# Performance work log

Measured on AMD Instinct MI355X. Metric: run time of the kernel, lower is better.

The kernel has to match this reference:

```python
import jax, jax.numpy as jnp
import numpy as np


def setup_inputs() -> dict:
    key = jax.random.key(0)
    k1, k2, k3 = jax.random.split(key, 3)
    B, T, N = 2, 16, 128
    INP, COND, OUT = 64, 64, 128
    x = jax.random.normal(k1, (B, T, N, INP), dtype=jnp.float32)
    cond = jax.random.normal(k2, (B, N, N, COND), dtype=jnp.float32)
    in_dim = 6 * INP + 2 * COND  # 512
    W = jax.random.normal(k3, (in_dim, OUT), dtype=jnp.float32) / np.sqrt(in_dim)
    b = jnp.zeros((OUT,), dtype=jnp.float32)
    return {"x": x, "cond": cond, "W": W, "b": b}


def reference(x, cond, W, b):
    # x: (B,T,N,C), cond: (B,N,N,Cc), W: (6C+2Cc, O), b: (O,)
    B, T, N, C = x.shape
    Cc = cond.shape[-1]
    # temporal boundary-zeroed copies (faithful to torch cat of zeros + slices)
    x1 = x.at[:, 0].set(0.0)        # zeros at t=0
    x2 = x.at[:, -1].set(0.0)       # zeros at t=T-1
    xc = jnp.concatenate([x1, x, x2], axis=-1)  # (B,T,N,3C)
    # decompose the big linear over the concat [x1_pair, x2_pair, cond1, cond2]
    W1 = W[: 3 * C]
    W2 = W[3 * C: 6 * C]
    Wc1 = W[6 * C: 6 * C + Cc]
    Wc2 = W[6 * C + Cc:]
    a = jnp.einsum('btnc,co->btno', xc, W1)               # n1 contribution
    bpart = jnp.einsum('btnc,co->btno', xc, W2)            # n2 contribution
    # cond1[b,t,i,j] = cond[b,i,j]; cond2[b,t,i,j] = cond[b,j,i]
    cpart = (jnp.einsum('bijc,co->bijo', cond, Wc1)
             + jnp.einsum('bjic,co->bijo', cond, Wc2))     # (B,N,N,O)
    s = (a[:, :, :, None, :] + bpart[:, :, None, :, :]
         + cpart[:, None, :, :, :] + b)                    # (B,T,N,N,O)
    act = s * jax.nn.sigmoid(s)                            # swish
    return jnp.max(act, axis=3)                            # amax over n2 -> (B,T,N,O)
```

## Files before the change

kernel.cpp:

```cpp
#include <hip/hip_runtime.h>
#include <math.h>

#define B_ 2
#define T_ 16
#define N_ 128
#define CI 64
#define CO 128

#define AQ_OFF 0
#define BT_OFF 524288
#define CQ_OFF 1048576

typedef __attribute__((ext_vector_type(8))) short short8;
typedef __attribute__((ext_vector_type(4))) float f32x4;

__device__ __forceinline__ float4 f4add(float4 a, float4 b) {
  return make_float4(a.x + b.x, a.y + b.y, a.z + b.z, a.w + b.w);
}
__device__ __forceinline__ float4 f4max(float4 a, float4 b) {
  return make_float4(fmaxf(a.x, b.x), fmaxf(a.y, b.y), fmaxf(a.z, b.z), fmaxf(a.w, b.w));
}
__device__ __forceinline__ float4 f4min(float4 a, float4 b) {
  return make_float4(fminf(a.x, b.x), fminf(a.y, b.y), fminf(a.z, b.z), fminf(a.w, b.w));
}
__device__ __forceinline__ void f4fma(float4& acc, float s, float4 v) {
  acc.x = fmaf(s, v.x, acc.x);
  acc.y = fmaf(s, v.y, acc.y);
  acc.z = fmaf(s, v.z, acc.z);
  acc.w = fmaf(s, v.w, acc.w);
}
__device__ __forceinline__ float silu1(float v) { return v / (1.0f + __expf(-v)); }
__device__ __forceinline__ float4 silu4(float4 v) {
  return make_float4(silu1(v.x), silu1(v.y), silu1(v.z), silu1(v.w));
}
__device__ __forceinline__ float4 shfl4x(float4 v, int m) {
  return make_float4(__shfl_xor(v.x, m, 64), __shfl_xor(v.y, m, 64),
                     __shfl_xor(v.z, m, 64), __shfl_xor(v.w, m, 64));
}
__device__ __forceinline__ unsigned int bf2(float a, float b) {
  unsigned int ua = __float_as_uint(a);
  unsigned int ub = __float_as_uint(b);
  ua = (ua + 0x7FFFu + ((ua >> 16) & 1u)) >> 16;
  ub = (ub + 0x7FFFu + ((ub >> 16) & 1u)) >> 16;
  return (ub << 16) | ua;
}
__device__ __forceinline__ uint4 pack8(float4 lo, float4 hi) {
  return make_uint4(bf2(lo.x, lo.y), bf2(lo.z, lo.w), bf2(hi.x, hi.y), bf2(hi.z, hi.w));
}

__global__ __launch_bounds__(256) void k_ab3(
    const float* __restrict__ x, const float* __restrict__ W,
    const float* __restrict__ bias, float* __restrict__ AQ, float* __restrict__ BT)
{
  __shared__ __align__(16) float WL[64 * 128];
  __shared__ float xT[64 * 17];

  int blk = blockIdx.x;
  int nq  = blk & 7;
  int dst = (blk >> 3) & 1;
  int t   = (blk >> 4) & 15;
  int b   = blk >> 8;
  float f0 = (t != 0)      ? 1.0f : 0.0f;
  float f2 = (t != T_ - 1) ? 1.0f : 0.0f;
  int tid = threadIdx.x;

  const float4* W4 = (const float4*)W;
  float4* WL4 = (float4*)WL;
  int wb = dst * 6144;
  #pragma unroll
  for (int k = 0; k < 8; k++) {
    int idx4 = tid + k * 256;
    float4 wa = W4[wb + idx4];
    float4 wm = W4[wb + 2048 + idx4];
    float4 wc = W4[wb + 4096 + idx4];
    WL4[idx4] = make_float4(f0 * wa.x + wm.x + f2 * wc.x,
                            f0 * wa.y + wm.y + f2 * wc.y,
                            f0 * wa.z + wm.z + f2 * wc.z,
                            f0 * wa.w + wm.w + f2 * wc.w);
  }
  {
    long xb = ((long)(b * T_ + t) * N_ + nq * 16) * CI;
    #pragma unroll
    for (int k = 0; k < 4; k++) {
      int idx = tid + k * 256;
      int c = idx & 63, n = idx >> 6;
      xT[c * 17 + n] = x[xb + n * CI + c];
    }
  }
  __syncthreads();

  int nl = tid & 15;
  int qg = tid >> 4;
  float4 acc0, acc1;
  if (dst == 0) {
    acc0 = ((const float4*)bias)[qg * 2];
    acc1 = ((const float4*)bias)[qg * 2 + 1];
  } else {
    acc0 = make_float4(0, 0, 0, 0); acc1 = acc0;
  }
  #pragma unroll 8
  for (int c = 0; c < 64; c++) {
    float xv = xT[c * 17 + nl];
    float4 w0 = WL4[c * 32 + qg * 2];
    float4 w1 = WL4[c * 32 + qg * 2 + 1];
    f4fma(acc0, xv, w0);
    f4fma(acc1, xv, w1);
  }
  int n = nq * 16 + nl;
  float4* dp4 = (float4*)(dst ? BT : AQ);
  int q0 = qg * 2, q1 = qg * 2 + 1;
  long i0 = (((long)(b * 8 + (q0 >> 2)) * 16 + t) * 128 + n) * 4 + (q0 & 3);
  long i1 = (((long)(b * 8 + (q1 >> 2)) * 16 + t) * 128 + n) * 4 + (q1 & 3);
  dp4[i0] = acc0;
  dp4[i1] = acc1;
}

__global__ __launch_bounds__(256) void k_cp4b(
    const float* __restrict__ cond, const float* __restrict__ W,
    float* __restrict__ CQ)
{
  __shared__ __align__(16) unsigned char smem[49152];
  uint4* AF  = (uint4*)smem;
  uint4* WcF = (uint4*)(smem + 16384);
  float* Cp  = (float*)smem;

  int blk = blockIdx.x;
  int jh = blk & 1;
  int i  = (blk >> 1) & 127;
  int b  = blk >> 8;
  int tid = threadIdx.x;

  #pragma unroll
  for (int f = 0; f < 8; f++) {
    int fid = tid + f * 256;
    int lane_f = fid & 63;
    int ot   = (fid >> 6) & 7;
    int kh   = (fid >> 9) & 1;
    int term = fid >> 10;
    int o  = ot * 16 + (lane_f & 15);
    int kb = kh * 32 + (lane_f >> 4) * 8;
    float v[8];
    #pragma unroll
    for (int u = 0; u < 8; u++)
      v[u] = W[(384 + term * 64 + kb + u) * 128 + o];
    WcF[fid] = pack8(make_float4(v[0], v[1], v[2], v[3]),
                     make_float4(v[4], v[5], v[6], v[7]));
  }
  #pragma unroll
  for (int k = 0; k < 4; k++) {
    int idx = tid + k * 256;
    int term = idx >> 9;
    int rem = idx & 511;
    int jl = rem >> 3, oct = rem & 7;
    long row = (term == 0) ? ((long)(b * N_ + i) * N_ + jh * 64 + jl)
                           : ((long)(b * N_ + jh * 64 + jl) * N_ + i);
    const float4* src = (const float4*)(cond + row * 64 + oct * 8);
    float4 lo = src[0], hi = src[1];
    int frag = term * 512 + ((jl >> 4) * 2 + (oct >> 2)) * 64 + (oct & 3) * 16 + (jl & 15);
    AF[frag] = pack8(lo, hi);
  }
  __syncthreads();

  int lane = tid & 63;
  int w    = tid >> 6;
  f32x4 acc[8];
  #pragma unroll
  for (int ot = 0; ot < 8; ot++) {
    acc[ot][0] = 0.f; acc[ot][1] = 0.f; acc[ot][2] = 0.f; acc[ot][3] = 0.f;
  }
  const short8* AF8 = (const short8*)AF;
  const short8* WF8 = (const short8*)WcF;
  #pragma unroll
  for (int term = 0; term < 2; term++) {
    #pragma unroll
    for (int kh = 0; kh < 2; kh++) {
      short8 a = AF8[term * 512 + (w * 2 + kh) * 64 + lane];
      #pragma unroll
      for (int ot = 0; ot < 8; ot++) {
        short8 bv = WF8[((term * 2 + kh) * 8 + ot) * 64 + lane];
        acc[ot] = __builtin_amdgcn_mfma_f32_16x16x32_bf16(a, bv, acc[ot], 0, 0, 0);
      }
    }
  }
  __syncthreads();

  {
    int col = lane & 15;
    int row0 = w * 16 + (lane >> 4) * 4;
    #pragma unroll
    for (int ot = 0; ot < 8; ot++) {
      f32x4 d = acc[ot];
      int cbase = ot * 16 + col;
      Cp[(row0 + 0) * 132 + cbase] = d[0];
      Cp[(row0 + 1) * 132 + cbase] = d[1];
      Cp[(row0 + 2) * 132 + cbase] = d[2];
      Cp[(row0 + 3) * 132 + cbase] = d[3];
    }
  }
  __syncthreads();

  {
    const float4* Cp4 = (const float4*)Cp;
    float4* CQ4 = (float4*)CQ;
    int oql = tid & 3;
    int jl  = (tid >> 2) & 63;
    #pragma unroll
    for (int of_l = 0; of_l < 8; of_l++) {
      CQ4[(((long)(b * 8 + of_l) * 128) + jh * 64 + jl) * 512 + i * 4 + oql] =
          Cp4[jl * 33 + of_l * 4 + oql];
    }
  }
}

__global__ __launch_bounds__(256, 1) void k_red7(
    const float* __restrict__ AQ, const float* __restrict__ BT,
    const float* __restrict__ CQ, float* __restrict__ out)
{
  __shared__ __align__(16) float4 BtL[8192];

  int blk = blockIdx.x;
  int ih = blk & 15;
  int of = (blk >> 4) & 7;
  int b  = blk >> 7;
  int tid = threadIdx.x;

  const float4* BT4 = (const float4*)BT;
  const float4* CQ4 = (const float4*)CQ;
  const float4* AQ4 = (const float4*)AQ;

  long btbase = (long)(b * 8 + of) * 8192;
  #pragma unroll
  for (int k = 0; k < 32; k++) BtL[tid + k * 256] = BT4[btbase + tid + k * 256];
  __syncthreads();

  int w    = tid >> 6;
  int lane = tid & 63;
  int jh = lane >> 5;
  int il = (lane >> 2) & 7;
  int oq = lane & 3;
  int jb = w * 32 + jh * 16;

  const float4* cq = CQ4 + ((long)(b * 8 + of) * 128) * 512 + (long)(ih * 8 + il) * 4 + oq;

  float4 mx[16], mn[16];
  #pragma unroll
  for (int t = 0; t < 16; t++) {
    mx[t] = make_float4(-3.4e38f, -3.4e38f, -3.4e38f, -3.4e38f);
    mn[t] = make_float4(3.4e38f, 3.4e38f, 3.4e38f, 3.4e38f);
  }

  #pragma unroll
  for (int jj = 0; jj < 16; jj += 4) {
    float4 c0 = cq[(long)(jb + jj + 0) * 512];
    float4 c1 = cq[(long)(jb + jj + 1) * 512];
    float4 c2 = cq[(long)(jb + jj + 2) * 512];
    float4 c3 = cq[(long)(jb + jj + 3) * 512];
    #pragma unroll
    for (int t = 0; t < 16; t++) {
      int bb = (t * 128 + jb + jj) * 4 + oq;
      float4 s0 = f4add(c0, BtL[bb]);
      float4 s1 = f4add(c1, BtL[bb + 4]);
      float4 s2 = f4add(c2, BtL[bb + 8]);
      float4 s3 = f4add(c3, BtL[bb + 12]);
      mx[t] = f4max(mx[t], f4max(f4max(s0, s1), f4max(s2, s3)));
      mn[t] = f4min(mn[t], f4min(f4min(s0, s1), f4min(s2, s3)));
    }
  }

  #pragma unroll
  for (int t = 0; t < 16; t++) {
    mx[t] = f4max(mx[t], shfl4x(mx[t], 32));
    mn[t] = f4min(mn[t], shfl4x(mn[t], 32));
  }

  __syncthreads();
  float4* scr = BtL;
  if (jh == 0) {
    #pragma unroll
    for (int t = 0; t < 16; t++) {
      int sidx = ((w * 16 + t) * 8 + il) * 4 + oq;
      scr[sidx]        = mx[t];
      scr[2048 + sidx] = mn[t];
    }
  }
  __syncthreads();

  #pragma unroll
  for (int r = 0; r < 2; r++) {
    int oid = tid + r * 256;
    int t   = oid >> 5;
    int il2 = (oid >> 2) & 7;
    int oq2 = oid & 3;
    int s0 = ((0 * 16 + t) * 8 + il2) * 4 + oq2;
    float4 MX = scr[s0];
    float4 MN = scr[2048 + s0];
    #pragma unroll
    for (int ww = 1; ww < 4; ww++) {
      int si = ((ww * 16 + t) * 8 + il2) * 4 + oq2;
      MX = f4max(MX, scr[si]);
      MN = f4min(MN, scr[2048 + si]);
    }
    float4 av = AQ4[(((long)(b * 8 + of) * 16 + t) * 128 + ih * 8 + il2) * 4 + oq2];
    float4 res = f4max(silu4(f4add(MX, av)), silu4(f4add(MN, av)));
    ((float4*)out)[((long)((b * 16 + t) * 128) + ih * 8 + il2) * 32 + of * 4 + oq2] = res;
  }
}

extern "C" void kernel_launch(void* const* d_in, const int* in_sizes, int n_in,
                              void* d_out, int out_size, void* d_ws, size_t ws_size,
                              hipStream_t stream) {
  const float* x    = (const float*)d_in[0];
  const float* cond = (const float*)d_in[1];
  const float* W    = (const float*)d_in[2];
  const float* bias = (const float*)d_in[3];
  float* out = (float*)d_out;

  float* ws = (float*)d_ws;
  float* AQ = ws + AQ_OFF;
  float* BT = ws + BT_OFF;
  float* CQ = ws + CQ_OFF;

  k_ab3<<<512, 256, 0, stream>>>(x, W, bias, AQ, BT);
  k_cp4b<<<512, 256, 0, stream>>>(cond, W, CQ);
  k_red7<<<256, 256, 0, stream>>>(AQ, BT, CQ, out);
}
```

Measured before the change: 107.4 us.

## Split reduction kernel over time halves to double grid and halve LDS

The max/min reduction kernel now splits the 16 timesteps into two halves per block, doubling the grid to 512 blocks and halving the shared-memory B tile to 64KB so two blocks can reside per CU. All 16 cond vectors per thread are preloaded into registers before the barrier, overlapping the global loads with the LDS fill. The trade-off is that each cond value is loaded twice, once per time-half block, and register pressure rises from holding 16 preloaded float4s.

```diff
diff --git a/kernel.cpp b/kernel.cpp
--- a/kernel.cpp
+++ b/kernel.cpp
@@ -212,26 +212,26 @@
   }
 }
 
-__global__ __launch_bounds__(256, 1) void k_red7(
+__global__ __launch_bounds__(256, 2) void k_red8(
     const float* __restrict__ AQ, const float* __restrict__ BT,
     const float* __restrict__ CQ, float* __restrict__ out)
 {
-  __shared__ __align__(16) float4 BtL[8192];
+  __shared__ __align__(16) float4 BtL[4096];
 
   int blk = blockIdx.x;
   int ih = blk & 15;
-  int of = (blk >> 4) & 7;
-  int b  = blk >> 7;
+  int th = (blk >> 4) & 1;
+  int of = (blk >> 5) & 7;
+  int b  = blk >> 8;
   int tid = threadIdx.x;
 
   const float4* BT4 = (const float4*)BT;
   const float4* CQ4 = (const float4*)CQ;
   const float4* AQ4 = (const float4*)AQ;
 
-  long btbase = (long)(b * 8 + of) * 8192;
-  #pragma unroll
-  for (int k = 0; k < 32; k++) BtL[tid + k * 256] = BT4[btbase + tid + k * 256];
-  __syncthreads();
+  long btbase = ((long)(b * 8 + of) * 16 + th * 8) * 512;
+  #pragma unroll
+  for (int k = 0; k < 16; k++) BtL[tid + k * 256] = BT4[btbase + tid + k * 256];
 
   int w    = tid >> 6;
   int lane = tid & 63;
@@ -242,64 +242,72 @@
 
   const float4* cq = CQ4 + ((long)(b * 8 + of) * 128) * 512 + (long)(ih * 8 + il) * 4 + oq;
 
-  float4 mx[16], mn[16];
-  #pragma unroll
-  for (int t = 0; t < 16; t++) {
+  float4 c[8], d[8];
+  #pragma unroll
+  for (int k = 0; k < 8; k++) c[k] = cq[(long)(jb + k) * 512];
+  #pragma unroll
+  for (int k = 0; k < 8; k++) d[k] = cq[(long)(jb + 8 + k) * 512];
+
+  __syncthreads();
+
+  float4 mx[8], mn[8];
+  #pragma unroll
+  for (int t = 0; t < 8; t++) {
     mx[t] = make_float4(-3.4e38f, -3.4e38f, -3.4e38f, -3.4e38f);
     mn[t] = make_float4(3.4e38f, 3.4e38f, 3.4e38f, 3.4e38f);
   }
 
   #pragma unroll
-  for (int jj = 0; jj < 16; jj += 4) {
-    float4 c0 = cq[(long)(jb + jj + 0) * 512];
-    float4 c1 = cq[(long)(jb + jj + 1) * 512];
-    float4 c2 = cq[(long)(jb + jj + 2) * 512];
-    float4 c3 = cq[(long)(jb + jj + 3) * 512];
-    #pragma unroll
-    for (int t = 0; t < 16; t++) {
-      int bb = (t * 128 + jb + jj) * 4 + oq;
-      float4 s0 = f4add(c0, BtL[bb]);
-      float4 s1 = f4add(c1, BtL[bb + 4]);
-      float4 s2 = f4add(c2, BtL[bb + 8]);
-      float4 s3 = f4add(c3, BtL[bb + 12]);
-      mx[t] = f4max(mx[t], f4max(f4max(s0, s1), f4max(s2, s3)));
-      mn[t] = f4min(mn[t], f4min(f4min(s0, s1), f4min(s2, s3)));
-    }
-  }
-
-  #pragma unroll
-  for (int t = 0; t < 16; t++) {
-    mx[t] = f4max(mx[t], shfl4x(mx[t], 32));
-    mn[t] = f4min(mn[t], shfl4x(mn[t], 32));
+  for (int k = 0; k < 8; k++) {
+    #pragma unroll
+    for (int tl = 0; tl < 8; tl++) {
+      float4 s = f4add(c[k], BtL[(tl * 128 + jb + k) * 4 + oq]);
+      mx[tl] = f4max(mx[tl], s);
+      mn[tl] = f4min(mn[tl], s);
+    }
+  }
+  #pragma unroll
+  for (int k = 0; k < 8; k++) {
+    #pragma unroll
+    for (int tl = 0; tl < 8; tl++) {
+      float4 s = f4add(d[k], BtL[(tl * 128 + jb + 8 + k) * 4 + oq]);
+      mx[tl] = f4max(mx[tl], s);
+      mn[tl] = f4min(mn[tl], s);
+    }
+  }
+
+  #pragma unroll
+  for (int tl = 0; tl < 8; tl++) {
+    mx[tl] = f4max(mx[tl], shfl4x(mx[tl], 32));
+    mn[tl] = f4min(mn[tl], shfl4x(mn[tl], 32));
   }
 
   __syncthreads();
   float4* scr = BtL;
   if (jh == 0) {
     #pragma unroll
-    for (int t = 0; t < 16; t++) {
-      int sidx = ((w * 16 + t) * 8 + il) * 4 + oq;
-      scr[sidx]        = mx[t];
-      scr[2048 + sidx] = mn[t];
-    }
-  }
-  __syncthreads();
-
-  #pragma unroll
-  for (int r = 0; r < 2; r++) {
-    int oid = tid + r * 256;
-    int t   = oid >> 5;
-    int il2 = (oid >> 2) & 7;
-    int oq2 = oid & 3;
-    int s0 = ((0 * 16 + t) * 8 + il2) * 4 + oq2;
+    for (int tl = 0; tl < 8; tl++) {
+      int sidx = ((w * 8 + tl) * 8 + il) * 4 + oq;
+      scr[sidx]        = mx[tl];
+      scr[1024 + sidx] = mn[tl];
+    }
+  }
+  __syncthreads();
+
+  {
+    int tl  = tid >> 5;
+    int il2 = (tid >> 2) & 7;
+    int oq2 = tid & 3;
+    int s0 = (tl * 8 + il2) * 4 + oq2;
     float4 MX = scr[s0];
-    float4 MN = scr[2048 + s0];
+    float4 MN = scr[1024 + s0];
     #pragma unroll
     for (int ww = 1; ww < 4; ww++) {
-      int si = ((ww * 16 + t) * 8 + il2) * 4 + oq2;
+      int si = ((ww * 8 + tl) * 8 + il2) * 4 + oq2;
       MX = f4max(MX, scr[si]);
-      MN = f4min(MN, scr[2048 + si]);
-    }
+      MN = f4min(MN, scr[1024 + si]);
+    }
+    int t = th * 8 + tl;
     float4 av = AQ4[(((long)(b * 8 + of) * 16 + t) * 128 + ih * 8 + il2) * 4 + oq2];
     float4 res = f4max(silu4(f4add(MX, av)), silu4(f4add(MN, av)));
     ((float4*)out)[((long)((b * 16 + t) * 128) + ih * 8 + il2) * 32 + of * 4 + oq2] = res;
@@ -322,5 +330,5 @@
 
   k_ab3<<<512, 256, 0, stream>>>(x, W, bias, AQ, BT);
   k_cp4b<<<512, 256, 0, stream>>>(cond, W, CQ);
-  k_red7<<<256, 256, 0, stream>>>(AQ, BT, CQ, out);
-}
+  k_red8<<<512, 256, 0, stream>>>(AQ, BT, CQ, out);
+}
```

Measured after the change: 93.96 us. 1.14x faster.
